# Performance work log

Measured on AMD Instinct MI355X. Metric: run time of the kernel, lower is better.

The kernel has to match this reference:

```python
import jax, jax.numpy as jnp
import numpy as np

N_NODES = 100000


def _gcn_conv(x, edge_index, W, b, n_nodes):
    """PyG GCNConv: add self-loops, symmetric deg^-1/2 normalization,
    linear transform, scatter-sum aggregation, bias."""
    loop = jnp.arange(n_nodes, dtype=edge_index.dtype)
    src = jnp.concatenate([edge_index[0], loop])  # message sources
    dst = jnp.concatenate([edge_index[1], loop])  # message targets
    deg = jax.ops.segment_sum(jnp.ones_like(dst, dtype=x.dtype), dst,
                              num_segments=n_nodes)
    dinv = jnp.where(deg > 0, jax.lax.rsqrt(jnp.maximum(deg, 1.0)), 0.0)
    norm = dinv[src] * dinv[dst]  # [E+N]
    h = x @ W  # [N, out] transform before aggregation (fewer bytes moved)
    msg = h[src] * norm[:, None]  # [E+N, out]
    out = jax.ops.segment_sum(msg, dst, num_segments=n_nodes)
    return out + b


def setup_inputs() -> dict:
    key = jax.random.key(0)
    k1, k2, k3, k4, k5, k6 = jax.random.split(key, 6)
    in_ch, hid, out_ch = 128, 64, 64
    x = jax.random.normal(k1, (N_NODES, in_ch), dtype=jnp.float32)
    edge_index = jax.random.randint(k2, (2, 3200000), 0, N_NODES, dtype=jnp.int64)
    # Glorot-style init for GCN weights, zeros for bias (PyG default)
    W1 = jax.random.normal(k3, (in_ch, hid), dtype=jnp.float32) / np.sqrt(in_ch)
    b1 = jnp.zeros((hid,), dtype=jnp.float32)
    W2 = jax.random.normal(k4, (hid, out_ch), dtype=jnp.float32) / np.sqrt(hid)
    b2 = jnp.zeros((out_ch,), dtype=jnp.float32)
    return {"x": x, "edge_index": edge_index, "W1": W1, "b1": b1,
            "W2": W2, "b2": b2}


def reference(x, edge_index, W1, b1, W2, b2):
    n = x.shape[0]
    h = _gcn_conv(x, edge_index, W1, b1, n)
    h = jax.nn.relu(h)
    out = _gcn_conv(h, edge_index, W2, b2, n)
    return out
```

## Files before the change

### kernel.cpp

```cpp
#include <hip/hip_runtime.h>
#include <math.h>


#define BKT_SHIFT 9
#define BKT_NODES 512
#define NBSH      256
#define CHUNK     8192
#define MAXB      20480
#define RSH       13
#define NBIN      8192

typedef unsigned short ushort_t;

static __device__ __forceinline__ unsigned short f2bf(float f) {
    unsigned u = __float_as_uint(f);
    unsigned r = (u + 0x7FFFu + ((u >> 16) & 1u)) >> 16;
    return (unsigned short)r;
}
static __device__ __forceinline__ float bf_lo(unsigned u) {
    return __uint_as_float(u << 16);
}
static __device__ __forceinline__ float bf_hi(unsigned u) {
    return __uint_as_float(u & 0xFFFF0000u);
}

struct ushort4_t { unsigned short x, y, z, w; };

__global__ __launch_bounds__(256) void coarse_hist(const int* __restrict__ dst,
                                                   int* __restrict__ bhist,
                                                   int E, int NB) {
    __shared__ int h[NBSH];
    const int t  = threadIdx.x;
    const int e0 = blockIdx.x * CHUNK;
    const int n  = min(CHUNK, E - e0);
    h[t] = 0;
    __syncthreads();
    for (int i = t; i < n; i += 256) atomicAdd(&h[dst[e0 + i] >> BKT_SHIFT], 1);
    __syncthreads();
    if (t < NB && h[t] > 0) atomicAdd(&bhist[t], h[t]);
}

__global__ __launch_bounds__(256) void scan196(const int* __restrict__ bhist,
                                               int* __restrict__ boffs,
                                               int* __restrict__ bcur, int NB, int E) {
    __shared__ int sh[256];
    int t = threadIdx.x;
    bcur[t] = 0;
    int orig = (t < NB) ? bhist[t] : 0;
    sh[t] = orig;
    __syncthreads();
    for (int d = 1; d < 256; d <<= 1) {
        int u = (t >= d) ? sh[t - d] : 0;
        __syncthreads();
        sh[t] += u;
        __syncthreads();
    }
    if (t < NB) boffs[t] = sh[t] - orig;
    if (t == NB) boffs[NB] = E;
    if (t == 255 && NB < 255) boffs[NB] = E;
}

__global__ __launch_bounds__(256) void bucket_bin(const int* __restrict__ src,
                                                  const int* __restrict__ dst,
                                                  const int* __restrict__ boffs,
                                                  int* __restrict__ bcur,
                                                  unsigned* __restrict__ pairs,
                                                  int E, int NB) {
    __shared__ unsigned stag[CHUNK];
    __shared__ int hist[NBSH];
    __shared__ int lofs[NBSH];
    __shared__ int lcur[NBSH];
    __shared__ int gbase[NBSH];
    const int t  = threadIdx.x;
    const int e0 = blockIdx.x * CHUNK;
    const int n  = min(CHUNK, E - e0);

    for (int i = t; i < NBSH; i += 256) hist[i] = 0;
    __syncthreads();
    for (int i = t; i < n; i += 256) atomicAdd(&hist[dst[e0 + i] >> BKT_SHIFT], 1);
    __syncthreads();
    int v = hist[t];
    lofs[t] = v;
    __syncthreads();
    for (int d = 1; d < 256; d <<= 1) {
        int u = (t >= d) ? lofs[t - d] : 0;
        __syncthreads();
        lofs[t] += u;
        __syncthreads();
    }
    if (t < NB) {
        lcur[t]  = lofs[t] - v;
        gbase[t] = (v > 0) ? boffs[t] + atomicAdd(&bcur[t], v) : 0;
    }
    __syncthreads();
    for (int i = t; i < n; i += 256) {
        int d = dst[e0 + i];
        int s = src[e0 + i];
        int b = d >> BKT_SHIFT;
        int p = atomicAdd(&lcur[b], 1);
        stag[p] = ((unsigned)(d & (BKT_NODES - 1)) << 17) | (unsigned)s;
    }
    __syncthreads();
    const int wv = t >> 6, ln = t & 63;
    for (int b = wv; b < NB; b += 4) {
        int cb = hist[b];
        if (cb == 0) continue;
        int lo = lofs[b] - cb;
        int gb = gbase[b];
        for (int i = ln; i < cb; i += 64) pairs[gb + i] = stag[lo + i];
    }
}

__global__ __launch_bounds__(1024) void csr_sort2(const unsigned* __restrict__ pairs,
                                                  const int* __restrict__ boffs,
                                                  unsigned* __restrict__ csr,
                                                  int* __restrict__ cnt,
                                                  int* __restrict__ offs,
                                                  float* __restrict__ dinv,
                                                  int N) {
    extern __shared__ unsigned st[];
    __shared__ int hist2[NBIN];
    __shared__ int sc[1024];
    const int b    = blockIdx.x;
    const int t    = threadIdx.x;
    const int n0   = b << BKT_SHIFT;
    const int base = boffs[b];
    const int ne   = boffs[b + 1] - base;

    for (int i = t; i < NBIN; i += 1024) hist2[i] = 0;
    __syncthreads();
    for (int i = t; i < ne; i += 1024) {
        unsigned p = pairs[base + i];
        int key = (int)(((p >> 17) << 4) | ((p & 0x1FFFFu) >> RSH));
        atomicAdd(&hist2[key], 1);
    }
    __syncthreads();
    if (t < BKT_NODES) {
        int node = n0 + t;
        if (node < N) {
            int d = 0;
#pragma unroll
            for (int r = 0; r < 16; ++r) d += hist2[(t << 4) + r];
            cnt[node]  = d;
            dinv[node] = rsqrtf((float)(d + 1));
        }
    }
    __syncthreads();
    int lv[8];
    int lsum = 0;
#pragma unroll
    for (int j = 0; j < 8; ++j) {
        int v = hist2[(t << 3) + j];
        lv[j] = v;
        lsum += v;
    }
    sc[t] = lsum;
    __syncthreads();
    for (int d = 1; d < 1024; d <<= 1) {
        int u = (t >= d) ? sc[t - d] : 0;
        __syncthreads();
        sc[t] += u;
        __syncthreads();
    }
    int run = sc[t] - lsum;
    __syncthreads();
#pragma unroll
    for (int j = 0; j < 8; ++j) {
        hist2[(t << 3) + j] = run;
        run += lv[j];
    }
    __syncthreads();
    if (t < BKT_NODES) {
        int node = n0 + t;
        if (node < N) offs[node] = base + hist2[t << 4];
    }
    __syncthreads();
    const bool fit = (ne <= MAXB);
    for (int i = t; i < ne; i += 1024) {
        unsigned p = pairs[base + i];
        int key = (int)(((p >> 17) << 4) | ((p & 0x1FFFFu) >> RSH));
        int pos = atomicAdd(&hist2[key], 1);
        unsigned sv = p & 0x1FFFFu;
        if (fit) st[pos] = sv;
        else     csr[base + pos] = sv;
    }
    if (fit) {
        __syncthreads();
        for (int i = t; i < ne; i += 1024) csr[base + i] = st[i];
    }
}

template <int K>
__global__ __launch_bounds__(256) void gemm_scale(const float* __restrict__ X,
                                                  const float* __restrict__ W,
                                                  const float* __restrict__ dinv,
                                                  ushort_t* __restrict__ G, int N) {
    __shared__ float Ws[K * 64];
    __shared__ float Xs[32][K + 1];
    const int t  = threadIdx.x;
    const int r0 = blockIdx.x * 32;

    for (int i = t; i < K * 16; i += 256)
        ((float4*)Ws)[i] = ((const float4*)W)[i];

    for (int i = t; i < 32 * (K / 4); i += 256) {
        int row = i / (K / 4);
        int kk  = (i % (K / 4)) * 4;
        int gr  = r0 + row;
        float4 v = make_float4(0.f, 0.f, 0.f, 0.f);
        if (gr < N) v = *(const float4*)(X + (size_t)gr * K + kk);
        Xs[row][kk + 0] = v.x; Xs[row][kk + 1] = v.y;
        Xs[row][kk + 2] = v.z; Xs[row][kk + 3] = v.w;
    }
    __syncthreads();

    const int cg = (t & 15) * 4;
    const int ry = t >> 4;
    float4 a0 = make_float4(0.f, 0.f, 0.f, 0.f);
    float4 a1 = make_float4(0.f, 0.f, 0.f, 0.f);
#pragma unroll 8
    for (int k = 0; k < K; ++k) {
        float4 w = *(const float4*)&Ws[k * 64 + cg];
        float x0 = Xs[ry][k];
        float x1 = Xs[ry + 16][k];
        a0.x = fmaf(x0, w.x, a0.x); a0.y = fmaf(x0, w.y, a0.y);
        a0.z = fmaf(x0, w.z, a0.z); a0.w = fmaf(x0, w.w, a0.w);
        a1.x = fmaf(x1, w.x, a1.x); a1.y = fmaf(x1, w.y, a1.y);
        a1.z = fmaf(x1, w.z, a1.z); a1.w = fmaf(x1, w.w, a1.w);
    }

    int row0 = r0 + ry;
    if (row0 < N) {
        float s = dinv[row0];
        ushort4_t o = { f2bf(a0.x * s), f2bf(a0.y * s), f2bf(a0.z * s), f2bf(a0.w * s) };
        *(ushort4_t*)(G + (size_t)row0 * 64 + cg) = o;
    }
    int row1 = r0 + ry + 16;
    if (row1 < N) {
        float s = dinv[row1];
        ushort4_t o = { f2bf(a1.x * s), f2bf(a1.y * s), f2bf(a1.z * s), f2bf(a1.w * s) };
        *(ushort4_t*)(G + (size_t)row1 * 64 + cg) = o;
    }
}

#define ACC8(v)                                         \
    acc[0] += bf_lo((v).x); acc[1] += bf_hi((v).x);     \
    acc[2] += bf_lo((v).y); acc[3] += bf_hi((v).y);     \
    acc[4] += bf_lo((v).z); acc[5] += bf_hi((v).z);     \
    acc[6] += bf_lo((v).w); acc[7] += bf_hi((v).w);

__global__ __launch_bounds__(256) void aggregate5(const ushort_t* __restrict__ G,
                                                  const int* __restrict__ offs,
                                                  const int* __restrict__ cnt,
                                                  const unsigned* __restrict__ csr,
                                                  const float* __restrict__ dinv,
                                                  const float* __restrict__ bias,
                                                  float* __restrict__ out, int N,
                                                  int do_relu) {
    int w    = (blockIdx.x * 256 + threadIdx.x) >> 6;
    int lane = threadIdx.x & 63;
    if (w >= N) return;
    const int grp = lane >> 3;
    const int sub = lane & 7;
    const int beg = offs[w];
    const int num = cnt[w];

    float acc[8] = {0.f, 0.f, 0.f, 0.f, 0.f, 0.f, 0.f, 0.f};
    if (grp == 0) {
        uint4 v = *(const uint4*)(G + (size_t)w * 64 + sub * 8);
        ACC8(v);
    }

    int e = 0;
    for (; e + 32 <= num; e += 32) {
        unsigned s0 = csr[beg + e + grp];
        unsigned s1 = csr[beg + e + 8 + grp];
        unsigned s2 = csr[beg + e + 16 + grp];
        unsigned s3 = csr[beg + e + 24 + grp];
        uint4 v0 = *(const uint4*)(G + ((size_t)s0 << 6) + (sub << 3));
        uint4 v1 = *(const uint4*)(G + ((size_t)s1 << 6) + (sub << 3));
        uint4 v2 = *(const uint4*)(G + ((size_t)s2 << 6) + (sub << 3));
        uint4 v3 = *(const uint4*)(G + ((size_t)s3 << 6) + (sub << 3));
        ACC8(v0); ACC8(v1); ACC8(v2); ACC8(v3);
    }
    if (e + 16 <= num) {
        unsigned s0 = csr[beg + e + grp];
        unsigned s1 = csr[beg + e + 8 + grp];
        uint4 v0 = *(const uint4*)(G + ((size_t)s0 << 6) + (sub << 3));
        uint4 v1 = *(const uint4*)(G + ((size_t)s1 << 6) + (sub << 3));
        ACC8(v0); ACC8(v1);
        e += 16;
    }
    if (e + 8 <= num) {
        unsigned s0 = csr[beg + e + grp];
        uint4 v0 = *(const uint4*)(G + ((size_t)s0 << 6) + (sub << 3));
        ACC8(v0);
        e += 8;
    }
    int rem = num - e;
    if (grp < rem) {
        unsigned s0 = csr[beg + e + grp];
        uint4 v0 = *(const uint4*)(G + ((size_t)s0 << 6) + (sub << 3));
        ACC8(v0);
    }

#pragma unroll
    for (int m = 8; m <= 32; m <<= 1) {
#pragma unroll
        for (int j = 0; j < 8; ++j) acc[j] += __shfl_xor(acc[j], m, 64);
    }

    if (grp == 0) {
        float d = dinv[w];
        float4 bl0 = *(const float4*)(bias + sub * 8);
        float4 bl1 = *(const float4*)(bias + sub * 8 + 4);
        float4 o0 = make_float4(fmaf(acc[0], d, bl0.x), fmaf(acc[1], d, bl0.y),
                                fmaf(acc[2], d, bl0.z), fmaf(acc[3], d, bl0.w));
        float4 o1 = make_float4(fmaf(acc[4], d, bl1.x), fmaf(acc[5], d, bl1.y),
                                fmaf(acc[6], d, bl1.z), fmaf(acc[7], d, bl1.w));
        if (do_relu) {
            o0.x = fmaxf(o0.x, 0.f); o0.y = fmaxf(o0.y, 0.f);
            o0.z = fmaxf(o0.z, 0.f); o0.w = fmaxf(o0.w, 0.f);
            o1.x = fmaxf(o1.x, 0.f); o1.y = fmaxf(o1.y, 0.f);
            o1.z = fmaxf(o1.z, 0.f); o1.w = fmaxf(o1.w, 0.f);
        }
        *(float4*)(out + (size_t)w * 64 + sub * 8)     = o0;
        *(float4*)(out + (size_t)w * 64 + sub * 8 + 4) = o1;
    }
}

extern "C" void kernel_launch(void* const* d_in, const int* in_sizes, int n_in,
                              void* d_out, int out_size, void* d_ws, size_t ws_size,
                              hipStream_t stream) {
    const float* x  = (const float*)d_in[0];
    const int*   ei = (const int*)d_in[1];
    const float* W1 = (const float*)d_in[2];
    const float* b1 = (const float*)d_in[3];
    const float* W2 = (const float*)d_in[4];
    const float* b2 = (const float*)d_in[5];
    float* out = (float*)d_out;

    const int IN_CH = 128;
    const int N = in_sizes[0] / IN_CH;
    const int E = in_sizes[1] / 2;
    const int* src = ei;
    const int* dst = ei + E;
    const int NB = (N + BKT_NODES - 1) >> BKT_SHIFT;

    char* ws = (char*)d_ws;
    size_t off = 0;
    auto take = [&](size_t bytes) -> char* {
        char* p = ws + off;
        off += (bytes + 255) & ~(size_t)255;
        return p;
    };
    float*    dinv  = (float*)take((size_t)N * 4);
    int*      cnt   = (int*)take((size_t)N * 4);
    int*      offs  = (int*)take((size_t)N * 4);
    int*      bhist = (int*)take(NBSH * 4);
    int*      boffs = (int*)take((NBSH + 1) * 4);
    int*      bcur  = (int*)take(NBSH * 4);
    unsigned* csr   = (unsigned*)take((size_t)E * 4);
    ushort_t* g     = (ushort_t*)take((size_t)E * 4);
    float*    a1    = (float*)take((size_t)N * 64 * 4);
    unsigned* pairs = (unsigned*)g;

    const int nbC = (E + CHUNK - 1) / CHUNK;

    hipMemsetAsync(bhist, 0, NBSH * 4, stream);
    coarse_hist<<<nbC, 256, 0, stream>>>(dst, bhist, E, NB);
    scan196<<<1, 256, 0, stream>>>(bhist, boffs, bcur, NB, E);
    bucket_bin<<<nbC, 256, 0, stream>>>(src, dst, boffs, bcur, pairs, E, NB);
    csr_sort2<<<NB, 1024, MAXB * 4, stream>>>(pairs, boffs, csr, cnt, offs, dinv, N);

    gemm_scale<128><<<(N + 31) / 32, 256, 0, stream>>>(x, W1, dinv, g, N);
    aggregate5<<<(N + 3) / 4, 256, 0, stream>>>(g, offs, cnt, csr, dinv, b1, a1, N, 1);
    gemm_scale<64><<<(N + 31) / 32, 256, 0, stream>>>(a1, W2, dinv, g, N);
    aggregate5<<<(N + 3) / 4, 256, 0, stream>>>(g, offs, cnt, csr, dinv, b2, out, N, 0);
}
```

Before: 337.5 us.

## Use fixed-capacity bucket slots and drop coarse histogram pass; register-tile GEMM

```diff
diff --git a/kernel.cpp b/kernel.cpp
--- a/kernel.cpp
+++ b/kernel.cpp
@@ -7,8 +7,6 @@
 #define NBSH      256
 #define CHUNK     8192
 #define MAXB      20480
-#define RSH       13
-#define NBIN      8192
 
 typedef unsigned short ushort_t;
 
@@ -26,43 +24,8 @@
 
 struct ushort4_t { unsigned short x, y, z, w; };
 
-__global__ __launch_bounds__(256) void coarse_hist(const int* __restrict__ dst,
-                                                   int* __restrict__ bhist,
-                                                   int E, int NB) {
-    __shared__ int h[NBSH];
-    const int t  = threadIdx.x;
-    const int e0 = blockIdx.x * CHUNK;
-    const int n  = min(CHUNK, E - e0);
-    h[t] = 0;
-    __syncthreads();
-    for (int i = t; i < n; i += 256) atomicAdd(&h[dst[e0 + i] >> BKT_SHIFT], 1);
-    __syncthreads();
-    if (t < NB && h[t] > 0) atomicAdd(&bhist[t], h[t]);
-}
-
-__global__ __launch_bounds__(256) void scan196(const int* __restrict__ bhist,
-                                               int* __restrict__ boffs,
-                                               int* __restrict__ bcur, int NB, int E) {
-    __shared__ int sh[256];
-    int t = threadIdx.x;
-    bcur[t] = 0;
-    int orig = (t < NB) ? bhist[t] : 0;
-    sh[t] = orig;
-    __syncthreads();
-    for (int d = 1; d < 256; d <<= 1) {
-        int u = (t >= d) ? sh[t - d] : 0;
-        __syncthreads();
-        sh[t] += u;
-        __syncthreads();
-    }
-    if (t < NB) boffs[t] = sh[t] - orig;
-    if (t == NB) boffs[NB] = E;
-    if (t == 255 && NB < 255) boffs[NB] = E;
-}
-
 __global__ __launch_bounds__(256) void bucket_bin(const int* __restrict__ src,
                                                   const int* __restrict__ dst,
-                                                  const int* __restrict__ boffs,
                                                   int* __restrict__ bcur,
                                                   unsigned* __restrict__ pairs,
                                                   int E, int NB) {
@@ -90,7 +53,7 @@
     }
     if (t < NB) {
         lcur[t]  = lofs[t] - v;
-        gbase[t] = (v > 0) ? boffs[t] + atomicAdd(&bcur[t], v) : 0;
+        gbase[t] = (v > 0) ? t * MAXB + atomicAdd(&bcur[t], v) : 0;
     }
     __syncthreads();
     for (int i = t; i < n; i += 256) {
@@ -107,87 +70,58 @@
         if (cb == 0) continue;
         int lo = lofs[b] - cb;
         int gb = gbase[b];
-        for (int i = ln; i < cb; i += 64) pairs[gb + i] = stag[lo + i];
-    }
-}
-
-__global__ __launch_bounds__(1024) void csr_sort2(const unsigned* __restrict__ pairs,
-                                                  const int* __restrict__ boffs,
-                                                  unsigned* __restrict__ csr,
-                                                  int* __restrict__ cnt,
-                                                  int* __restrict__ offs,
-                                                  float* __restrict__ dinv,
-                                                  int N) {
+        int lim = min(cb, (b + 1) * MAXB - gb);
+        for (int i = ln; i < lim; i += 64) pairs[gb + i] = stag[lo + i];
+    }
+}
+
+__global__ __launch_bounds__(1024) void csr_sort(const unsigned* __restrict__ pairs,
+                                                 const int* __restrict__ bcur,
+                                                 unsigned* __restrict__ csr,
+                                                 int* __restrict__ cnt,
+                                                 int* __restrict__ offs,
+                                                 float* __restrict__ dinv, int N) {
     extern __shared__ unsigned st[];
-    __shared__ int hist2[NBIN];
-    __shared__ int sc[1024];
+    __shared__ int h[BKT_NODES];
+    __shared__ int sc[BKT_NODES];
+    __shared__ int cur[BKT_NODES];
     const int b    = blockIdx.x;
     const int t    = threadIdx.x;
     const int n0   = b << BKT_SHIFT;
-    const int base = boffs[b];
-    const int ne   = boffs[b + 1] - base;
-
-    for (int i = t; i < NBIN; i += 1024) hist2[i] = 0;
+    const int base = b * MAXB;
+    const int ne   = min(bcur[b], MAXB);
+
+    if (t < BKT_NODES) h[t] = 0;
+    __syncthreads();
+    for (int i = t; i < ne; i += 1024) atomicAdd(&h[pairs[base + i] >> 17], 1);
+    __syncthreads();
+    int v = 0;
+    if (t < BKT_NODES) { v = h[t]; sc[t] = v; }
+    __syncthreads();
+    for (int d = 1; d < BKT_NODES; d <<= 1) {
+        int u = (t < BKT_NODES && t >= d) ? sc[t - d] : 0;
+        __syncthreads();
+        if (t < BKT_NODES) sc[t] += u;
+        __syncthreads();
+    }
+    if (t < BKT_NODES) {
+        int ex = sc[t] - v;
+        cur[t] = ex;
+        int node = n0 + t;
+        if (node < N) {
+            cnt[node]  = v;
+            offs[node] = base + ex;
+            dinv[node] = rsqrtf((float)(v + 1));
+        }
+    }
     __syncthreads();
     for (int i = t; i < ne; i += 1024) {
         unsigned p = pairs[base + i];
-        int key = (int)(((p >> 17) << 4) | ((p & 0x1FFFFu) >> RSH));
-        atomicAdd(&hist2[key], 1);
-    }
-    __syncthreads();
-    if (t < BKT_NODES) {
-        int node = n0 + t;
-        if (node < N) {
-            int d = 0;
-#pragma unroll
-            for (int r = 0; r < 16; ++r) d += hist2[(t << 4) + r];
-            cnt[node]  = d;
-            dinv[node] = rsqrtf((float)(d + 1));
-        }
-    }
-    __syncthreads();
-    int lv[8];
-    int lsum = 0;
-#pragma unroll
-    for (int j = 0; j < 8; ++j) {
-        int v = hist2[(t << 3) + j];
-        lv[j] = v;
-        lsum += v;
-    }
-    sc[t] = lsum;
-    __syncthreads();
-    for (int d = 1; d < 1024; d <<= 1) {
-        int u = (t >= d) ? sc[t - d] : 0;
-        __syncthreads();
-        sc[t] += u;
-        __syncthreads();
-    }
-    int run = sc[t] - lsum;
-    __syncthreads();
-#pragma unroll
-    for (int j = 0; j < 8; ++j) {
-        hist2[(t << 3) + j] = run;
-        run += lv[j];
-    }
-    __syncthreads();
-    if (t < BKT_NODES) {
-        int node = n0 + t;
-        if (node < N) offs[node] = base + hist2[t << 4];
-    }
-    __syncthreads();
-    const bool fit = (ne <= MAXB);
-    for (int i = t; i < ne; i += 1024) {
-        unsigned p = pairs[base + i];
-        int key = (int)(((p >> 17) << 4) | ((p & 0x1FFFFu) >> RSH));
-        int pos = atomicAdd(&hist2[key], 1);
-        unsigned sv = p & 0x1FFFFu;
-        if (fit) st[pos] = sv;
-        else     csr[base + pos] = sv;
-    }
-    if (fit) {
-        __syncthreads();
-        for (int i = t; i < ne; i += 1024) csr[base + i] = st[i];
-    }
+        int pos = atomicAdd(&cur[p >> 17], 1);
+        st[pos] = p & 0x1FFFFu;
+    }
+    __syncthreads();
+    for (int i = t; i < ne; i += 1024) csr[base + i] = st[i];
 }
 
 template <int K>
@@ -196,50 +130,58 @@
                                                   const float* __restrict__ dinv,
                                                   ushort_t* __restrict__ G, int N) {
     __shared__ float Ws[K * 64];
-    __shared__ float Xs[32][K + 1];
     const int t  = threadIdx.x;
-    const int r0 = blockIdx.x * 32;
+    const int r0 = blockIdx.x * 128;
 
     for (int i = t; i < K * 16; i += 256)
         ((float4*)Ws)[i] = ((const float4*)W)[i];
 
-    for (int i = t; i < 32 * (K / 4); i += 256) {
-        int row = i / (K / 4);
-        int kk  = (i % (K / 4)) * 4;
-        int gr  = r0 + row;
-        float4 v = make_float4(0.f, 0.f, 0.f, 0.f);
-        if (gr < N) v = *(const float4*)(X + (size_t)gr * K + kk);
-        Xs[row][kk + 0] = v.x; Xs[row][kk + 1] = v.y;
-        Xs[row][kk + 2] = v.z; Xs[row][kk + 3] = v.w;
-    }
-    __syncthreads();
-
     const int cg = (t & 15) * 4;
-    const int ry = t >> 4;
-    float4 a0 = make_float4(0.f, 0.f, 0.f, 0.f);
-    float4 a1 = make_float4(0.f, 0.f, 0.f, 0.f);
-#pragma unroll 8
-    for (int k = 0; k < K; ++k) {
-        float4 w = *(const float4*)&Ws[k * 64 + cg];
-        float x0 = Xs[ry][k];
-        float x1 = Xs[ry + 16][k];
-        a0.x = fmaf(x0, w.x, a0.x); a0.y = fmaf(x0, w.y, a0.y);
-        a0.z = fmaf(x0, w.z, a0.z); a0.w = fmaf(x0, w.w, a0.w);
-        a1.x = fmaf(x1, w.x, a1.x); a1.y = fmaf(x1, w.y, a1.y);
-        a1.z = fmaf(x1, w.z, a1.z); a1.w = fmaf(x1, w.w, a1.w);
-    }
-
-    int row0 = r0 + ry;
-    if (row0 < N) {
-        float s = dinv[row0];
-        ushort4_t o = { f2bf(a0.x * s), f2bf(a0.y * s), f2bf(a0.z * s), f2bf(a0.w * s) };
-        *(ushort4_t*)(G + (size_t)row0 * 64 + cg) = o;
-    }
-    int row1 = r0 + ry + 16;
-    if (row1 < N) {
-        float s = dinv[row1];
-        ushort4_t o = { f2bf(a1.x * s), f2bf(a1.y * s), f2bf(a1.z * s), f2bf(a1.w * s) };
-        *(ushort4_t*)(G + (size_t)row1 * 64 + cg) = o;
+    const int rb = r0 + (t >> 4) * 8;
+
+    float acc[8][4];
+#pragma unroll
+    for (int j = 0; j < 8; ++j) {
+        acc[j][0] = 0.f; acc[j][1] = 0.f; acc[j][2] = 0.f; acc[j][3] = 0.f;
+    }
+    __syncthreads();
+
+    const bool full = (rb + 8 <= N);
+    for (int k = 0; k < K; k += 4) {
+        float4 xr[8];
+        if (full) {
+#pragma unroll
+            for (int j = 0; j < 8; ++j)
+                xr[j] = *(const float4*)(X + (size_t)(rb + j) * K + k);
+        } else {
+#pragma unroll
+            for (int j = 0; j < 8; ++j)
+                xr[j] = (rb + j < N) ? *(const float4*)(X + (size_t)(rb + j) * K + k)
+                                     : make_float4(0.f, 0.f, 0.f, 0.f);
+        }
+#pragma unroll
+        for (int kk = 0; kk < 4; ++kk) {
+            float4 w = *(const float4*)&Ws[(k + kk) * 64 + cg];
+#pragma unroll
+            for (int j = 0; j < 8; ++j) {
+                float xv = (&xr[j].x)[kk];
+                acc[j][0] = fmaf(xv, w.x, acc[j][0]);
+                acc[j][1] = fmaf(xv, w.y, acc[j][1]);
+                acc[j][2] = fmaf(xv, w.z, acc[j][2]);
+                acc[j][3] = fmaf(xv, w.w, acc[j][3]);
+            }
+        }
+    }
+
+#pragma unroll
+    for (int j = 0; j < 8; ++j) {
+        int row = rb + j;
+        if (row < N) {
+            float s = dinv[row];
+            ushort4_t o = { f2bf(acc[j][0] * s), f2bf(acc[j][1] * s),
+                            f2bf(acc[j][2] * s), f2bf(acc[j][3] * s) };
+            *(ushort4_t*)(G + (size_t)row * 64 + cg) = o;
+        }
     }
 }
 
@@ -357,24 +299,20 @@
     float*    dinv  = (float*)take((size_t)N * 4);
     int*      cnt   = (int*)take((size_t)N * 4);
     int*      offs  = (int*)take((size_t)N * 4);
-    int*      bhist = (int*)take(NBSH * 4);
-    int*      boffs = (int*)take((NBSH + 1) * 4);
     int*      bcur  = (int*)take(NBSH * 4);
-    unsigned* csr   = (unsigned*)take((size_t)E * 4);
-    ushort_t* g     = (ushort_t*)take((size_t)E * 4);
+    unsigned* csr   = (unsigned*)take((size_t)NB * MAXB * 4);
+    ushort_t* g     = (ushort_t*)take((size_t)N * 64 * 2);
     float*    a1    = (float*)take((size_t)N * 64 * 4);
-    unsigned* pairs = (unsigned*)g;
+    unsigned* pairs = (unsigned*)a1;
 
     const int nbC = (E + CHUNK - 1) / CHUNK;
 
-    hipMemsetAsync(bhist, 0, NBSH * 4, stream);
-    coarse_hist<<<nbC, 256, 0, stream>>>(dst, bhist, E, NB);
-    scan196<<<1, 256, 0, stream>>>(bhist, boffs, bcur, NB, E);
-    bucket_bin<<<nbC, 256, 0, stream>>>(src, dst, boffs, bcur, pairs, E, NB);
-    csr_sort2<<<NB, 1024, MAXB * 4, stream>>>(pairs, boffs, csr, cnt, offs, dinv, N);
-
-    gemm_scale<128><<<(N + 31) / 32, 256, 0, stream>>>(x, W1, dinv, g, N);
+    hipMemsetAsync(bcur, 0, NBSH * 4, stream);
+    bucket_bin<<<nbC, 256, 0, stream>>>(src, dst, bcur, pairs, E, NB);
+    csr_sort<<<NB, 1024, MAXB * 4, stream>>>(pairs, bcur, csr, cnt, offs, dinv, N);
+
+    gemm_scale<128><<<(N + 127) / 128, 256, 0, stream>>>(x, W1, dinv, g, N);
     aggregate5<<<(N + 3) / 4, 256, 0, stream>>>(g, offs, cnt, csr, dinv, b1, a1, N, 1);
-    gemm_scale<64><<<(N + 31) / 32, 256, 0, stream>>>(a1, W2, dinv, g, N);
+    gemm_scale<64><<<(N + 127) / 128, 256, 0, stream>>>(a1, W2, dinv, g, N);
     aggregate5<<<(N + 3) / 4, 256, 0, stream>>>(g, offs, cnt, csr, dinv, b2, out, N, 0);
 }
```

Result: no change. 332.5 us (-1.5%).
